# Performance work log

Measured on AMD Instinct MI355X. Metric: run time of the kernel, lower is better.

The kernel has to match this reference:

```python
import jax, jax.numpy as jnp
import numpy as np

N = 4096       # nodes
NFEAT = 256    # feature dim
NCLASS = 16
E = 65536      # edges = N * avg_degree(16)
NLAYER = 4
ALPHA = 0.5    # blancealpha (non-trainable)
LAMBDA_1 = 1.0
LAMBDA_2 = 1.0
EPS = 1e-12    # F.normalize eps


def setup_inputs() -> dict:
    key = jax.random.key(0)
    ks = jax.random.split(key, 9)
    feat = jax.random.normal(ks[0], (N, NFEAT), dtype=jnp.float32)
    z0 = jax.random.uniform(ks[1], (N, NFEAT), dtype=jnp.float32)       # torch.rand init of z
    w1 = jax.random.uniform(ks[2], (N, N), dtype=jnp.float32)           # uniform_(0,1)
    EA = jax.random.uniform(ks[3], (N, N), dtype=jnp.float32)           # uniform_(0,1)
    w2_w = jax.random.normal(ks[4], (2 * NFEAT, NCLASS), dtype=jnp.float32) * 0.05
    w2_b = jnp.zeros((NCLASS,), dtype=jnp.float32)
    edge_i = jax.random.randint(ks[5], (E,), 0, N, dtype=jnp.int32)
    edge_j = jax.random.randint(ks[6], (E,), 0, N, dtype=jnp.int32)
    edge_val = jax.random.uniform(ks[7], (E,), dtype=jnp.float32)
    # dense adjacency from the sparse edge list (coalesce -> duplicate indices sum)
    adj = jnp.zeros((N, N), dtype=jnp.float32).at[edge_i, edge_j].add(edge_val)
    # w22 = ones with zeros at edge positions (as in __init__)
    w22 = jnp.ones((N, N), dtype=jnp.float32).at[edge_i, edge_j].set(0.0)
    return dict(feat=feat, z0=z0, w1=w1, EA=EA, w2_w=w2_w, w2_b=w2_b,
                adj=adj, w22=w22, edge_val=edge_val, edge_i=edge_i, edge_j=edge_j)


def reference(feat, z0, w1, EA, w2_w, w2_b, adj, w22, edge_val, edge_i, edge_j):
    n = feat.shape[0]
    y = feat                      # y starts as feat
    z = z0                        # torch.rand init, passed in for determinism
    EP = jnp.ones((n, n), dtype=feat.dtype)
    masked_EA = ALPHA * EA * w22  # constant across layers
    for _ in range(NLAYER):
        # dropout is identity in eval mode (training=False)
        A = adj * EP + masked_EA            # [n, n]
        yyT = y @ y.T                       # [n, n] (reused; same values as the two torch.mm calls)
        temp = EP.T @ y + A @ y - yyT @ y   # [n, nfeat]
        temp = jax.nn.sigmoid(w1 @ temp)
        y_n = (LAMBDA_2 / 2) * temp + feat
        z_n = z - A @ z                     # (I - A) @ z
        # ans(z, adj): edgewise ||z_i - z_j|| * adj_val scattered to dense
        P = jnp.linalg.norm(z[edge_i] - z[edge_j], axis=1) * edge_val   # [E]
        M = jnp.zeros((n, n), dtype=z.dtype).at[edge_i, edge_j].add(P)
        EP = (LAMBDA_2 * (yyT - masked_EA) - LAMBDA_1 * 0.5 * M) / LAMBDA_2
        y, z = y_n, z_n
    # F.normalize(p=2, dim=1)
    y = y / jnp.maximum(jnp.linalg.norm(y, axis=1, keepdims=True), EPS)
    z = z / jnp.maximum(jnp.linalg.norm(z, axis=1, keepdims=True), EPS)
    p = jnp.concatenate([z, y], axis=1)     # [n, 2*nfeat]
    logits = p @ w2_w + w2_b
    return jax.nn.log_softmax(logits, axis=1)
```

## Files before the change

kernel.cpp:

```cpp
#include <hip/hip_runtime.h>

#define Nn 4096
#define Ff 256
#define NCLS 16
#define Ne 65536
#define TSZ 262144
#define NF (Nn*Ff)
#define NNx (Nn*Nn)
#define KS 8

typedef unsigned short u16;
typedef unsigned int u32;
typedef __attribute__((ext_vector_type(8))) short short8;
typedef __attribute__((ext_vector_type(4))) float float4v;

__device__ __forceinline__ float bfh(u16 u){ return __uint_as_float(((u32)u)<<16); }
__device__ __forceinline__ u16 f2bf(float f){
    u32 u = __float_as_uint(f);
    return (u16)((u + 0x7FFFu + ((u>>16)&1u)) >> 16);
}
__device__ __forceinline__ void gload16(const u16* g, u16* l){
    __builtin_amdgcn_global_load_lds(
        (const __attribute__((address_space(1))) u32*)(const void*)g,
        (__attribute__((address_space(3))) u32*)(void*)l, 16, 0, 0);
}

__device__ float g_yA[NF], g_yB[NF], g_zA[NF], g_zB[NF], g_t1[NF], g_T1[NF];
__device__ float g_G[Ff*Ff], g_col[Ff], g_P[Ne], g_cc[Ne], g_hV[TSZ];
__device__ float g_pb[(size_t)KS*NF];
__device__ u32 g_hK[TSZ], g_slot[Ne];
__device__ int g_cntI[Nn], g_cntJ[Nn], g_rpI[Nn+1], g_rpJ[Nn+1], g_fI[Nn], g_fJ[Nn];
__device__ int g_lI[Ne], g_lJ[Ne];
__device__ __align__(16) u16 g_w1h[NNx], g_w1l[NNx];
__device__ __align__(16) u16 g_meh[NNx], g_mel[NNx];
__device__ __align__(16) u16 g_mth[NNx], g_mtl[NNx];
__device__ __align__(16) u16 g_xAh[NF], g_xAl[NF];
__device__ __align__(16) u16 g_xBh[NF], g_xBl[NF];
__device__ __align__(16) u16 g_x2h[NF], g_x2l[NF];
__device__ __align__(16) u16 g_yhA[NF], g_ylA[NF];
__device__ __align__(16) u16 g_yhB[NF], g_ylB[NF];
__device__ __align__(16) u16 g_gth[Ff*Ff], g_gtl[Ff*Ff];

__global__ __launch_bounds__(256) void k_copy(float* dst, const float* src, int n){
    int i = blockIdx.x*256 + threadIdx.x;
    if (i < n) dst[i] = src[i];
}
__global__ __launch_bounds__(256) void k_zero(float* p, int n){
    int i = blockIdx.x*256 + threadIdx.x;
    if (i < n) p[i] = 0.f;
}
__global__ __launch_bounds__(256) void k_zeroi(int* p, int n){
    int i = blockIdx.x*256 + threadIdx.x;
    if (i < n) p[i] = 0;
}
__global__ __launch_bounds__(256) void k_fillc(float* p, float v, int n){
    int i = blockIdx.x*256 + threadIdx.x;
    if (i < n) p[i] = v;
}
__global__ __launch_bounds__(256) void k_hkeys_clear(u32* K){
    int i = blockIdx.x*256 + threadIdx.x;
    if (i < TSZ) K[i] = 0xFFFFFFFFu;
}
__global__ __launch_bounds__(256) void k_hsetup(u32* K, u32* slot, const int* ei, const int* ej){
    int e = blockIdx.x*256 + threadIdx.x;
    if (e >= Ne) return;
    u32 key = ((u32)ei[e] << 12) | (u32)ej[e];
    u32 h = (key * 2654435761u) & (TSZ-1);
    for (;;){
        u32 old = atomicCAS(&K[h], 0xFFFFFFFFu, key);
        if (old == 0xFFFFFFFFu || old == key){ slot[e] = h; break; }
        h = (h+1) & (TSZ-1);
    }
}
__global__ __launch_bounds__(256) void k_hacc(float* V, const float* P, const u32* slot){
    int e = blockIdx.x*256 + threadIdx.x;
    if (e < Ne) atomicAdd(&V[slot[e]], P[e]);
}

__global__ __launch_bounds__(256) void k_count(int* cntI, int* cntJ, const int* ei, const int* ej){
    int e = blockIdx.x*256 + threadIdx.x;
    if (e < Ne){ atomicAdd(&cntI[ei[e]], 1); atomicAdd(&cntJ[ej[e]], 1); }
}
__global__ __launch_bounds__(1024) void k_scan(const int* cnt, int* rp){
    __shared__ int s[1024];
    int t = threadIdx.x, b = t*4;
    int a0 = cnt[b], a1 = cnt[b+1], a2 = cnt[b+2], a3 = cnt[b+3];
    int sum = a0+a1+a2+a3;
    s[t] = sum; __syncthreads();
    for (int o = 1; o < 1024; o <<= 1){
        int v = (t >= o) ? s[t-o] : 0;
        __syncthreads();
        s[t] += v;
        __syncthreads();
    }
    int excl = s[t] - sum;
    rp[b] = excl; rp[b+1] = excl+a0; rp[b+2] = excl+a0+a1; rp[b+3] = excl+a0+a1+a2;
    if (t == 1023) rp[4096] = s[1023];
}
__global__ __launch_bounds__(256) void k_fillcsr(const int* rpI, const int* rpJ, int* fI, int* fJ,
                                                 int* lI, int* lJ, const int* ei, const int* ej){
    int e = blockIdx.x*256 + threadIdx.x;
    if (e >= Ne) return;
    int i = ei[e], j = ej[e];
    lI[rpI[i] + atomicAdd(&fI[i], 1)] = e;
    lJ[rpJ[j] + atomicAdd(&fJ[j], 1)] = e;
}

__global__ __launch_bounds__(256) void k_split(u16* hi, u16* lo, const float* w){
    int i = blockIdx.x*256 + threadIdx.x;
    float v = w[i];
    u16 h = f2bf(v); hi[i] = h; lo[i] = f2bf(v - bfh(h));
}
__global__ __launch_bounds__(256) void k_splitME2(u16* meh, u16* mel, u16* mth, u16* mtl,
                                                  const float* ea, const float* w22){
    __shared__ float T[64][65];
    int r0 = blockIdx.y*64, c0 = blockIdx.x*64;
    int c = threadIdx.x & 63, rr = threadIdx.x >> 6;
    for (int q = 0; q < 16; ++q){
        int r = q*4 + rr;
        size_t idx = (size_t)(r0+r)*Nn + c0 + c;
        float v = 0.5f*ea[idx]*w22[idx];
        T[r][c] = v;
        u16 h = f2bf(v); meh[idx] = h; mel[idx] = f2bf(v - bfh(h));
    }
    __syncthreads();
    for (int q = 0; q < 16; ++q){
        int r = q*4 + rr;
        float v = T[c][r];
        size_t o = (size_t)(c0+r)*Nn + r0 + c;
        u16 h = f2bf(v); mth[o] = h; mtl[o] = f2bf(v - bfh(h));
    }
}
__global__ __launch_bounds__(256) void k_splitXT(u16* hi, u16* lo, const float* X){
    __shared__ float T[64][65];
    int r0 = blockIdx.y*64, c0 = blockIdx.x*64;
    int c = threadIdx.x & 63, rr = threadIdx.x >> 6;
    for (int q = 0; q < 16; ++q){
        int r = q*4 + rr;
        T[r][c] = X[(size_t)(r0+r)*Ff + c0 + c];
    }
    __syncthreads();
    for (int q = 0; q < 16; ++q){
        int r = q*4 + rr;
        float v = T[c][r];
        size_t o = (size_t)(c0+r)*Nn + r0 + c;
        u16 h = f2bf(v); hi[o] = h; lo[o] = f2bf(v - bfh(h));
    }
}
__global__ __launch_bounds__(256) void k_splitGT(u16* hi, u16* lo, const float* Gm){
    __shared__ float T[64][65];
    int r0 = blockIdx.y*64, c0 = blockIdx.x*64;
    int c = threadIdx.x & 63, rr = threadIdx.x >> 6;
    for (int q = 0; q < 16; ++q){
        int r = q*4 + rr;
        T[r][c] = Gm[(r0+r)*Ff + c0 + c];
    }
    __syncthreads();
    for (int q = 0; q < 16; ++q){
        int r = q*4 + rr;
        float v = T[c][r];
        int o = (c0+r)*Ff + r0 + c;
        u16 h = f2bf(v); hi[o] = h; lo[o] = f2bf(v - bfh(h));
    }
}

__device__ __forceinline__ void mm_tile(
    const u16* __restrict__ Ahp, const u16* __restrict__ Alp,
    const u16* __restrict__ Bhp, const u16* __restrict__ Blp,
    size_t sA, size_t sB, int i0, int j0, int k0,
    u16* LAh, u16* LAl, u16* LBh, u16* LBl,
    float4v* acc, int lane, int w)
{
    const int g1 = w*64 + lane;
    const int g2 = g1 + 256;
    const int r1 = g1>>3, p1 = g1&7, r2 = g2>>3, p2 = g2&7;
    const size_t a1 = (size_t)(i0+r1)*sA + (size_t)(k0 + ((p1 ^ (r1&7))<<3));
    const size_t a2 = (size_t)(i0+r2)*sA + (size_t)(k0 + ((p2 ^ (r2&7))<<3));
    const size_t b1 = (size_t)(j0+r1)*sB + (size_t)(k0 + ((p1 ^ (r1&7))<<3));
// ... 12 lines not shown
    const int aswz = arow & 7;
    #pragma unroll
    for (int kk = 0; kk < 2; ++kk){
        const int ch = kk*4 + (lane>>4);
        short8 ah = *(const short8*)(LAh + arow*64 + ((ch ^ aswz)<<3));
        short8 al = *(const short8*)(LAl + arow*64 + ((ch ^ aswz)<<3));
        #pragma unroll
        for (int c = 0; c < 4; ++c){
            const int brow = c*16 + (lane&15);
            const int bo = brow*64 + ((ch ^ (brow&7))<<3);
            short8 bh = *(const short8*)(LBh + bo);
            short8 bl = *(const short8*)(LBl + bo);
            acc[c] = __builtin_amdgcn_mfma_f32_16x16x32_bf16(ah, bh, acc[c], 0,0,0);
            acc[c] = __builtin_amdgcn_mfma_f32_16x16x32_bf16(ah, bl, acc[c], 0,0,0);
            acc[c] = __builtin_amdgcn_mfma_f32_16x16x32_bf16(al, bh, acc[c], 0,0,0);
        }
    }
}

template<int V>
__global__ __launch_bounds__(256) void k_mm(float* __restrict__ out,
        const u16* __restrict__ Ahp, const u16* __restrict__ Alp,
        const u16* __restrict__ Bhp, const u16* __restrict__ Blp,
        size_t sA, size_t sB, int nkt,
        const float* __restrict__ aux1){
    __shared__ u16 LAh[4096], LAl[4096], LBh[4096], LBl[4096];
    const int tid = threadIdx.x, lane = tid & 63, w = tid >> 6;
    const int j0 = blockIdx.x*64, i0 = blockIdx.y*64;
    float4v acc[4];
    #pragma unroll
    for (int c = 0; c < 4; ++c) acc[c] = (float4v){0.f,0.f,0.f,0.f};
    for (int kt = 0; kt < nkt; ++kt)
        mm_tile(Ahp, Alp, Bhp, Blp, sA, sB, i0, j0, kt*64, LAh, LAl, LBh, LBl, acc, lane, w);
    #pragma unroll
    for (int c = 0; c < 4; ++c)
        #pragma unroll
        for (int r = 0; r < 4; ++r){
            int grow = i0 + w*16 + (lane>>4)*4 + r;
            int gcol = j0 + c*16 + (lane&15);
            size_t idx = (size_t)grow*Ff + gcol;
            float v = acc[c][r];
            if constexpr (V == 3) out[idx] = aux1[idx] - v;
            if constexpr (V == 4) out[idx] = aux1[gcol] - v;
            if constexpr (V == 5) out[idx] = v;
        }
}

__global__ __launch_bounds__(256) void k_gram_mm(float* __restrict__ G,
        const u16* __restrict__ Ahp, const u16* __restrict__ Alp,
        const u16* __restrict__ Bhp, const u16* __restrict__ Blp){
    __shared__ u16 LAh[4096], LAl[4096], LBh[4096], LBl[4096];
    const int tid = threadIdx.x, lane = tid & 63, w = tid >> 6;
    const int j0 = blockIdx.x*64, i0 = blockIdx.y*64, kb = blockIdx.z*256;
    float4v acc[4];
    #pragma unroll
    for (int c = 0; c < 4; ++c) acc[c] = (float4v){0.f,0.f,0.f,0.f};
    for (int kt = 0; kt < 4; ++kt)
        mm_tile(Ahp, Alp, Bhp, Blp, (size_t)Nn, (size_t)Nn, i0, j0, kb + kt*64, LAh, LAl, LBh, LBl, acc, lane, w);
    #pragma unroll
    for (int c = 0; c < 4; ++c)
        #pragma unroll
        for (int r = 0; r < 4; ++r){
            int grow = i0 + w*16 + (lane>>4)*4 + r;
            int gcol = j0 + c*16 + (lane&15);
            atomicAdd(&G[grow*Ff + gcol], acc[c][r]);
        }
}

__global__ __launch_bounds__(512) void k_mmB(float* __restrict__ pb,
        const u16* __restrict__ Ahp, const u16* __restrict__ Alp,
        const u16* __restrict__ Bhp, const u16* __restrict__ Blp){
    __shared__ u16 LAh[4096], LAl[4096], LBh[16384], LBl[16384];
    const int tid = threadIdx.x, lane = tid & 63, w = tid >> 6;
    const int z = blockIdx.x, i0 = blockIdx.y*64;
    const int wr = w >> 2, wc = w & 3;
    float4v acc[2][4];
    #pragma unroll
    for (int m = 0; m < 2; ++m)
        #pragma unroll
        for (int n = 0; n < 4; ++n) acc[m][n] = (float4v){0.f,0.f,0.f,0.f};

    const int ra = tid >> 3, pa = tid & 7;
    const size_t aoff = (size_t)(i0+ra)*Nn + (size_t)((pa ^ (ra&7))<<3);

    for (int kt = 0; kt < 8; ++kt){
        const int k0 = z*512 + kt*64;
        __syncthreads();
        gload16(Ahp + aoff + k0, LAh + tid*8);
        gload16(Alp + aoff + k0, LAl + tid*8);
        #pragma unroll
        for (int it = 0; it < 4; ++it){
            int g = it*512 + tid;
            int r = g >> 3, p = g & 7;
            size_t b = (size_t)r*Nn + (size_t)(k0 + ((p ^ (r&7))<<3));
            gload16(Bhp + b, LBh + g*8);
            gload16(Blp + b, LBl + g*8);
        }
        __syncthreads();
        #pragma unroll
        for (int kk = 0; kk < 2; ++kk){
            const int ch = kk*4 + (lane>>4);
            short8 ah0, ah1, al0, al1;
            {
                const int arow = wr*32 + (lane&15);
                const int ao = arow*64 + ((ch ^ (arow&7))<<3);
                ah0 = *(const short8*)(LAh + ao);
                al0 = *(const short8*)(LAl + ao);
            }
            {
                const int arow = wr*32 + 16 + (lane&15);
                const int ao = arow*64 + ((ch ^ (arow&7))<<3);
                ah1 = *(const short8*)(LAh + ao);
                al1 = *(const short8*)(LAl + ao);
            }
            #pragma unroll
            for (int n = 0; n < 4; ++n){
                const int bcol = wc*64 + n*16 + (lane&15);
                const int bo = bcol*64 + ((ch ^ (bcol&7))<<3);
                short8 bh = *(const short8*)(LBh + bo);
                short8 bl = *(const short8*)(LBl + bo);
                acc[0][n] = __builtin_amdgcn_mfma_f32_16x16x32_bf16(ah0, bh, acc[0][n], 0,0,0);
                acc[0][n] = __builtin_amdgcn_mfma_f32_16x16x32_bf16(ah0, bl, acc[0][n], 0,0,0);
                acc[0][n] = __builtin_amdgcn_mfma_f32_16x16x32_bf16(al0, bh, acc[0][n], 0,0,0);
                acc[1][n] = __builtin_amdgcn_mfma_f32_16x16x32_bf16(ah1, bh, acc[1][n], 0,0,0);
                acc[1][n] = __builtin_amdgcn_mfma_f32_16x16x32_bf16(ah1, bl, acc[1][n], 0,0,0);
                acc[1][n] = __builtin_amdgcn_mfma_f32_16x16x32_bf16(al1, bh, acc[1][n], 0,0,0);
            }
        }
    }
    float* op = pb + (size_t)z*NF;
    #pragma unroll
    for (int m = 0; m < 2; ++m)
        #pragma unroll
        for (int n = 0; n < 4; ++n)
            #pragma unroll
            for (int r = 0; r < 4; ++r){
                int row = i0 + wr*32 + m*16 + (lane>>4)*4 + r;
                int col = wc*64 + n*16 + (lane&15);
                op[(size_t)row*Ff + col] = acc[m][n][r];
            }
}

template<int V>
__global__ __launch_bounds__(256) void k_red(float* __restrict__ out, const float* __restrict__ pb,
                                             const float* __restrict__ aux, u16* __restrict__ oh,
                                             u16* __restrict__ ol){
    size_t i = (size_t)blockIdx.x*256 + threadIdx.x;
    float s = 0.f;
    #pragma unroll
    for (int zz = 0; zz < KS; ++zz) s += pb[(size_t)zz*NF + i];
    if constexpr (V == 0) out[i] += s;
    if constexpr (V == 1) out[i] -= s;
    if constexpr (V == 2){
        float v = aux[i] + 0.5f*(1.f/(1.f+expf(-s)));
        out[i] = v;
        u16 h = f2bf(v); oh[i] = h; ol[i] = f2bf(v - bfh(h));
    }
    if constexpr (V == 3) out[i] = aux[i] - s;
}

__global__ __launch_bounds__(256) void k_csrT(float* __restrict__ t1, const float* __restrict__ y,
        const float* __restrict__ cc, const float* __restrict__ P,
        const int* __restrict__ rpI, const int* __restrict__ lI, const int* __restrict__ ej,
        const int* __restrict__ rpJ, const int* __restrict__ lJ, const int* __restrict__ ei,
        int useM){
    const int r = blockIdx.x, f = threadIdx.x;
    float acc = 0.f;
    const int b0 = rpI[r], b1 = rpI[r+1];
    for (int p = b0; p < b1; ++p){
        int e = lI[p];
        acc += cc[e] * y[(size_t)ej[e]*Ff + f];
    }
    if (useM){
        const int c0 = rpJ[r], c1 = rpJ[r+1];
        for (int p = c0; p < c1; ++p){
            int e = lJ[p];
            acc -= 0.5f * P[e] * y[(size_t)ei[e]*Ff + f];
        }
    }
    t1[(size_t)r*Ff + f] += acc;
}
__global__ __launch_bounds__(256) void k_csrZ(float* __restrict__ zn, const float* __restrict__ z,
        const float* __restrict__ cc,
        const int* __restrict__ rpI, const int* __restrict__ lI, const int* __restrict__ ej){
    const int r = blockIdx.x, f = threadIdx.x;
    float acc = 0.f;
    const int b0 = rpI[r], b1 = rpI[r+1];
    for (int p = b0; p < b1; ++p){
        int e = lI[p];
        acc += cc[e] * z[(size_t)ej[e]*Ff + f];
    }
    zn[(size_t)r*Ff + f] -= acc;
}

__global__ __launch_bounds__(256) void k_colsum(float* col, const float* __restrict__ y){
    int j = threadIdx.x;
    int r0 = blockIdx.x*64;
    float s = 0.f;
    for (int i = 0; i < 64; ++i) s += y[(size_t)(r0+i)*Ff + j];
    atomicAdd(&col[j], s);
}

__global__ __launch_bounds__(256) void k_p(float* __restrict__ P, const float* __restrict__ z,
        const int* __restrict__ ei, const int* __restrict__ ej, const float* __restrict__ ev){
    int e = blockIdx.x*4 + (threadIdx.x >> 6);
    int lane = threadIdx.x & 63;
    int i = ei[e], j = ej[e];
    float s = 0.f;
    #pragma unroll
    for (int q = 0; q < 4; ++q){
        int f = lane + q*64;
        float d = z[(size_t)i*Ff + f] - z[(size_t)j*Ff + f];
        s += d*d;
    }
    #pragma unroll
    for (int o = 32; o; o >>= 1) s += __shfl_xor(s, o);
    if (lane == 0) P[e] = sqrtf(s) * ev[e];
}
__global__ __launch_bounds__(256) void k_ep(float* __restrict__ c, const float* __restrict__ y,
        const int* __restrict__ ei, const int* __restrict__ ej, const float* __restrict__ ev,
        const float* __restrict__ V, const u32* __restrict__ slot){
    int e = blockIdx.x*4 + (threadIdx.x >> 6);
    int lane = threadIdx.x & 63;
    int i = ei[e], j = ej[e];
    float s = 0.f;
    #pragma unroll
    for (int q = 0; q < 4; ++q){
        int f = lane + q*64;
        s += y[(size_t)i*Ff + f] * y[(size_t)j*Ff + f];
    }
    #pragma unroll
    for (int o = 32; o; o >>= 1) s += __shfl_xor(s, o);
    if (lane == 0) c[e] = ev[e] * (s - 0.5f * V[slot[e]]);
}

__global__ __launch_bounds__(256) void k_head(float* __restrict__ out, const float* __restrict__ y,
                                              const float* __restrict__ z, const float* __restrict__ w2w,
                                              const float* __restrict__ w2b){
    const int node = blockIdx.x, t = threadIdx.x;
    float yv = y[(size_t)node*Ff + t], zv = z[(size_t)node*Ff + t];
// ... 46 lines not shown
                              void* d_out, int out_size, void* d_ws, size_t ws_size,
                              hipStream_t stream){
    const float* feat = (const float*)d_in[0];
    const float* z0i  = (const float*)d_in[1];
    const float* w1p  = (const float*)d_in[2];
    const float* EAp  = (const float*)d_in[3];
    const float* w2w  = (const float*)d_in[4];
    const float* w2b  = (const float*)d_in[5];
    const float* w22p = (const float*)d_in[7];
    const float* evp  = (const float*)d_in[8];
    const int* ei   = (const int*)d_in[9];
    const int* ej   = (const int*)d_in[10];
    float* out = (float*)d_out;

    int ok = (n_in == 11) && (out_size == Nn*NCLS)
           && in_sizes[0]==NF && in_sizes[1]==NF && in_sizes[2]==NNx && in_sizes[3]==NNx
           && in_sizes[4]==2*Ff*NCLS && in_sizes[5]==NCLS && in_sizes[6]==NNx && in_sizes[7]==NNx
           && in_sizes[8]==Ne && in_sizes[9]==Ne && in_sizes[10]==Ne;
    if (!ok){
        k_fillc<<<(out_size+255)/256, 256, 0, stream>>>(out, -100.0f, out_size);
        return;
    }

    float *yA,*yB,*zA,*zB,*t1,*T1,*G,*col,*P,*cc,*hV,*pb; u32 *hK,*slot;
    int *cntI,*cntJ,*rpI,*rpJ,*fI,*fJ,*lI,*lJ;
    u16 *w1h,*w1l,*meh,*mel,*mth,*mtl,*xAh,*xAl,*xBh,*xBl,*x2h,*x2l,*yhA,*ylA,*yhB,*ylB,*gth,*gtl;
    hipGetSymbolAddress((void**)&yA,  HIP_SYMBOL(g_yA));
    hipGetSymbolAddress((void**)&yB,  HIP_SYMBOL(g_yB));
    hipGetSymbolAddress((void**)&zA,  HIP_SYMBOL(g_zA));
    hipGetSymbolAddress((void**)&zB,  HIP_SYMBOL(g_zB));
    hipGetSymbolAddress((void**)&t1,  HIP_SYMBOL(g_t1));
    hipGetSymbolAddress((void**)&T1,  HIP_SYMBOL(g_T1));
    hipGetSymbolAddress((void**)&G,   HIP_SYMBOL(g_G));
    hipGetSymbolAddress((void**)&col, HIP_SYMBOL(g_col));
    hipGetSymbolAddress((void**)&P,   HIP_SYMBOL(g_P));
    hipGetSymbolAddress((void**)&cc,  HIP_SYMBOL(g_cc));
    hipGetSymbolAddress((void**)&hV,  HIP_SYMBOL(g_hV));
    hipGetSymbolAddress((void**)&pb,  HIP_SYMBOL(g_pb));
    hipGetSymbolAddress((void**)&hK,  HIP_SYMBOL(g_hK));
    hipGetSymbolAddress((void**)&slot,HIP_SYMBOL(g_slot));
    hipGetSymbolAddress((void**)&cntI,HIP_SYMBOL(g_cntI));
    hipGetSymbolAddress((void**)&cntJ,HIP_SYMBOL(g_cntJ));
    hipGetSymbolAddress((void**)&rpI, HIP_SYMBOL(g_rpI));
    hipGetSymbolAddress((void**)&rpJ, HIP_SYMBOL(g_rpJ));
    hipGetSymbolAddress((void**)&fI,  HIP_SYMBOL(g_fI));
    hipGetSymbolAddress((void**)&fJ,  HIP_SYMBOL(g_fJ));
    hipGetSymbolAddress((void**)&lI,  HIP_SYMBOL(g_lI));
    hipGetSymbolAddress((void**)&lJ,  HIP_SYMBOL(g_lJ));
    hipGetSymbolAddress((void**)&w1h, HIP_SYMBOL(g_w1h));
    hipGetSymbolAddress((void**)&w1l, HIP_SYMBOL(g_w1l));
    hipGetSymbolAddress((void**)&meh, HIP_SYMBOL(g_meh));
    hipGetSymbolAddress((void**)&mel, HIP_SYMBOL(g_mel));
    hipGetSymbolAddress((void**)&mth, HIP_SYMBOL(g_mth));
    hipGetSymbolAddress((void**)&mtl, HIP_SYMBOL(g_mtl));
    hipGetSymbolAddress((void**)&xAh, HIP_SYMBOL(g_xAh));
    hipGetSymbolAddress((void**)&xAl, HIP_SYMBOL(g_xAl));
    hipGetSymbolAddress((void**)&xBh, HIP_SYMBOL(g_xBh));
    hipGetSymbolAddress((void**)&xBl, HIP_SYMBOL(g_xBl));
    hipGetSymbolAddress((void**)&x2h, HIP_SYMBOL(g_x2h));
    hipGetSymbolAddress((void**)&x2l, HIP_SYMBOL(g_x2l));
    hipGetSymbolAddress((void**)&yhA, HIP_SYMBOL(g_yhA));
    hipGetSymbolAddress((void**)&ylA, HIP_SYMBOL(g_ylA));
    hipGetSymbolAddress((void**)&yhB, HIP_SYMBOL(g_yhB));
    hipGetSymbolAddress((void**)&ylB, HIP_SYMBOL(g_ylB));
    hipGetSymbolAddress((void**)&gth, HIP_SYMBOL(g_gth));
    hipGetSymbolAddress((void**)&gtl, HIP_SYMBOL(g_gtl));

    const dim3 gG(Ff/64, Nn/64);
    const dim3 gXT(Ff/64, Nn/64);
    const dim3 gME(Nn/64, Nn/64);
    const dim3 gGT(Ff/64, Ff/64);
    const dim3 gGram(4, 4, 16);
    const dim3 gB(KS, Nn/64);

    k_split  <<<NNx/256, 256, 0, stream>>>(w1h, w1l, w1p);
    k_splitME2<<<gME, 256, 0, stream>>>(meh, mel, mth, mtl, EAp, w22p);
    k_copy<<<NF/256, 256, 0, stream>>>(yA, feat, NF);
    k_copy<<<NF/256, 256, 0, stream>>>(zA, z0i, NF);
    k_copy<<<Ne/256, 256, 0, stream>>>(cc, evp, Ne);
    k_split  <<<NF/256, 256, 0, stream>>>(yhA, ylA, yA);
    k_splitXT<<<gXT, 256, 0, stream>>>(xAh, xAl, yA);
    k_hkeys_clear<<<TSZ/256, 256, 0, stream>>>(hK);
    k_hsetup<<<Ne/256, 256, 0, stream>>>(hK, slot, ei, ej);
    k_zeroi<<<Nn/256, 256, 0, stream>>>(cntI, Nn);
    k_zeroi<<<Nn/256, 256, 0, stream>>>(cntJ, Nn);
    k_count<<<Ne/256, 256, 0, stream>>>(cntI, cntJ, ei, ej);
    k_scan<<<1, 1024, 0, stream>>>(cntI, rpI);
    k_scan<<<1, 1024, 0, stream>>>(cntJ, rpJ);
    k_zeroi<<<Nn/256, 256, 0, stream>>>(fI, Nn);
    k_zeroi<<<Nn/256, 256, 0, stream>>>(fJ, Nn);
    k_fillcsr<<<Ne/256, 256, 0, stream>>>(rpI, rpJ, fI, fJ, lI, lJ, ei, ej);

    float *y = yA, *yn = yB, *z = zA, *zn = zB;
    for (int t = 1; t <= 4; ++t){
        k_zero<<<Ff*Ff/256, 256, 0, stream>>>(G, Ff*Ff);
        k_gram_mm<<<gGram, 256, 0, stream>>>(G, xAh, xAl, xAh, xAl);
        k_splitGT<<<gGT, 256, 0, stream>>>(gth, gtl, G);
        if (t == 1){
            k_zero<<<1, 256, 0, stream>>>(col, Ff);
            k_colsum<<<64, 256, 0, stream>>>(col, y);
            k_mm<4><<<gG, 256, 0, stream>>>(t1, yhA, ylA, gth, gtl, (size_t)Ff, (size_t)Ff, 4, col);
        } else {
            k_mm<3><<<gG, 256, 0, stream>>>(t1, yhA, ylA, gth, gtl, (size_t)Ff, (size_t)Ff, 4, T1);
        }
        k_csrT<<<Nn, 256, 0, stream>>>(t1, y, cc, P, rpI, lI, ej, rpJ, lJ, ei, (t >= 2) ? 1 : 0);
        k_mmB<<<gB, 512, 0, stream>>>(pb, meh, mel, xAh, xAl);
        k_red<0><<<NF/256, 256, 0, stream>>>(t1, pb, nullptr, nullptr, nullptr);
        if (t >= 2){
            k_mmB<<<gB, 512, 0, stream>>>(pb, mth, mtl, xAh, xAl);
            k_red<1><<<NF/256, 256, 0, stream>>>(t1, pb, nullptr, nullptr, nullptr);
        }
        k_splitXT<<<gXT, 256, 0, stream>>>(x2h, x2l, t1);
        k_mmB<<<gB, 512, 0, stream>>>(pb, w1h, w1l, x2h, x2l);
        k_red<2><<<NF/256, 256, 0, stream>>>(yn, pb, feat, yhB, ylB);
        k_splitXT<<<gXT, 256, 0, stream>>>(x2h, x2l, z);
        k_mmB<<<gB, 512, 0, stream>>>(pb, meh, mel, x2h, x2l);
        k_red<3><<<NF/256, 256, 0, stream>>>(zn, pb, z, nullptr, nullptr);
        k_csrZ<<<Nn, 256, 0, stream>>>(zn, z, cc, rpI, lI, ej);
        if (t < 4){
            k_p<<<Ne/4, 256, 0, stream>>>(P, z, ei, ej, evp);
            k_zero<<<TSZ/256, 256, 0, stream>>>(hV, TSZ);
            k_hacc<<<Ne/256, 256, 0, stream>>>(hV, P, slot);
            k_ep<<<Ne/4, 256, 0, stream>>>(cc, y, ei, ej, evp, hV, slot);
            k_splitXT<<<gXT, 256, 0, stream>>>(xBh, xBl, yn);
            k_zero<<<Ff*Ff/256, 256, 0, stream>>>(G, Ff*Ff);
            k_gram_mm<<<gGram, 256, 0, stream>>>(G, xAh, xAl, xBh, xBl);
            k_splitGT<<<gGT, 256, 0, stream>>>(gth, gtl, G);
            k_mm<5><<<gG, 256, 0, stream>>>(T1, yhA, ylA, gth, gtl, (size_t)Ff, (size_t)Ff, 4, nullptr);
        }
        float* tmp;
        tmp = y; y = yn; yn = tmp;
        tmp = z; z = zn; zn = tmp;
        u16* tu;
        tu = xAh; xAh = xBh; xBh = tu;
        tu = xAl; xAl = xBl; xBl = tu;
        tu = yhA; yhA = yhB; yhB = tu;
        tu = ylA; ylA = ylB; ylB = tu;
    }
    k_head<<<Nn, 256, 0, stream>>>(out, y, z, w2w, w2b);
}
```

Baseline: 1.368 ms.

## Retile big GEMM with double-buffered 128x128 tiles and fuse reductions with splits

Rewrites the large N×N-by-N×F GEMM kernel to use 128x128 output tiles with double-buffered LDS staging and a split-K of 4 instead of 8. This cuts LDS reloads of the N×N operand and the partial-buffer traffic. Several other changes come with it. The reduction kernels now also do the transposed bf16 hi/lo split, and the z and y CSR passes are fused into one kernel. The Gram matrix is written as per-slice partials summed during the split, removing atomics and zeroing. Copies are dropped, and the init splits are vectorized with float4. Larger tiles mean fewer blocks and more LDS per block, so occupancy may drop.

```diff
diff --git a/kernel.cpp b/kernel.cpp
--- a/kernel.cpp
+++ b/kernel.cpp
@@ -7,7 +7,7 @@
 #define TSZ 262144
 #define NF (Nn*Ff)
 #define NNx (Nn*Nn)
-#define KS 8
+#define KS 4
 
 typedef unsigned short u16;
 typedef unsigned int u32;
@@ -26,7 +26,7 @@
 }
 
 __device__ float g_yA[NF], g_yB[NF], g_zA[NF], g_zB[NF], g_t1[NF], g_T1[NF];
-__device__ float g_G[Ff*Ff], g_col[Ff], g_P[Ne], g_cc[Ne], g_hV[TSZ];
+__device__ float g_Gp[16*Ff*Ff], g_col[Ff], g_P[Ne], g_cc[Ne], g_hV[TSZ];
 __device__ float g_pb[(size_t)KS*NF];
 __device__ u32 g_hK[TSZ], g_slot[Ne];
 __device__ int g_cntI[Nn], g_cntJ[Nn], g_rpI[Nn+1], g_rpJ[Nn+1], g_fI[Nn], g_fJ[Nn];
@@ -34,17 +34,12 @@
 __device__ __align__(16) u16 g_w1h[NNx], g_w1l[NNx];
 __device__ __align__(16) u16 g_meh[NNx], g_mel[NNx];
 __device__ __align__(16) u16 g_mth[NNx], g_mtl[NNx];
-__device__ __align__(16) u16 g_xAh[NF], g_xAl[NF];
-__device__ __align__(16) u16 g_xBh[NF], g_xBl[NF];
-__device__ __align__(16) u16 g_x2h[NF], g_x2l[NF];
-__device__ __align__(16) u16 g_yhA[NF], g_ylA[NF];
-__device__ __align__(16) u16 g_yhB[NF], g_ylB[NF];
+__device__ __align__(16) u16 g_x0h[NF], g_x0l[NF], g_x1h[NF], g_x1l[NF];
+__device__ __align__(16) u16 g_zt0h[NF], g_zt0l[NF], g_zt1h[NF], g_zt1l[NF];
+__device__ __align__(16) u16 g_yr0h[NF], g_yr0l[NF], g_yr1h[NF], g_yr1l[NF];
+__device__ __align__(16) u16 g_tth[NF], g_ttl[NF];
 __device__ __align__(16) u16 g_gth[Ff*Ff], g_gtl[Ff*Ff];
 
-__global__ __launch_bounds__(256) void k_copy(float* dst, const float* src, int n){
-    int i = blockIdx.x*256 + threadIdx.x;
-    if (i < n) dst[i] = src[i];
-}
 __global__ __launch_bounds__(256) void k_zero(float* p, int n){
     int i = blockIdx.x*256 + threadIdx.x;
     if (i < n) p[i] = 0.f;
@@ -71,10 +66,6 @@
         if (old == 0xFFFFFFFFu || old == key){ slot[e] = h; break; }
         h = (h+1) & (TSZ-1);
     }
-}
-__global__ __launch_bounds__(256) void k_hacc(float* V, const float* P, const u32* slot){
-    int e = blockIdx.x*256 + threadIdx.x;
-    if (e < Ne) atomicAdd(&V[slot[e]], P[e]);
 }
 
 __global__ __launch_bounds__(256) void k_count(int* cntI, int* cntJ, const int* ei, const int* ej){
@@ -106,29 +97,47 @@
     lJ[rpJ[j] + atomicAdd(&fJ[j], 1)] = e;
 }
 
-__global__ __launch_bounds__(256) void k_split(u16* hi, u16* lo, const float* w){
+__global__ __launch_bounds__(256) void k_split4(ushort4* hi, ushort4* lo, const float4* w, int n4){
     int i = blockIdx.x*256 + threadIdx.x;
-    float v = w[i];
-    u16 h = f2bf(v); hi[i] = h; lo[i] = f2bf(v - bfh(h));
+    if (i >= n4) return;
+    float4 v = w[i];
+    ushort4 h, l;
+    h.x = f2bf(v.x); l.x = f2bf(v.x - bfh(h.x));
+    h.y = f2bf(v.y); l.y = f2bf(v.y - bfh(h.y));
+    h.z = f2bf(v.z); l.z = f2bf(v.z - bfh(h.z));
+    h.w = f2bf(v.w); l.w = f2bf(v.w - bfh(h.w));
+    hi[i] = h; lo[i] = l;
 }
 __global__ __launch_bounds__(256) void k_splitME2(u16* meh, u16* mel, u16* mth, u16* mtl,
                                                   const float* ea, const float* w22){
     __shared__ float T[64][65];
     int r0 = blockIdx.y*64, c0 = blockIdx.x*64;
-    int c = threadIdx.x & 63, rr = threadIdx.x >> 6;
-    for (int q = 0; q < 16; ++q){
-        int r = q*4 + rr;
-        size_t idx = (size_t)(r0+r)*Nn + c0 + c;
-        float v = 0.5f*ea[idx]*w22[idx];
-        T[r][c] = v;
-        u16 h = f2bf(v); meh[idx] = h; mel[idx] = f2bf(v - bfh(h));
-    }
-    __syncthreads();
-    for (int q = 0; q < 16; ++q){
-        int r = q*4 + rr;
-        float v = T[c][r];
-        size_t o = (size_t)(c0+r)*Nn + r0 + c;
-        u16 h = f2bf(v); mth[o] = h; mtl[o] = f2bf(v - bfh(h));
+    int c4 = threadIdx.x & 15, rr = threadIdx.x >> 4;
+    for (int q = 0; q < 4; ++q){
+        int r = q*16 + rr;
+        size_t idx = (size_t)(r0+r)*Nn + c0 + c4*4;
+        float4 e4 = *(const float4*)(ea + idx);
+        float4 w4 = *(const float4*)(w22 + idx);
+        float v0 = 0.5f*e4.x*w4.x, v1 = 0.5f*e4.y*w4.y, v2 = 0.5f*e4.z*w4.z, v3 = 0.5f*e4.w*w4.w;
+        ushort4 h, l;
+        h.x = f2bf(v0); l.x = f2bf(v0 - bfh(h.x));
+        h.y = f2bf(v1); l.y = f2bf(v1 - bfh(h.y));
+        h.z = f2bf(v2); l.z = f2bf(v2 - bfh(h.z));
+        h.w = f2bf(v3); l.w = f2bf(v3 - bfh(h.w));
+        *(ushort4*)(meh + idx) = h; *(ushort4*)(mel + idx) = l;
+        T[r][c4*4+0] = v0; T[r][c4*4+1] = v1; T[r][c4*4+2] = v2; T[r][c4*4+3] = v3;
+    }
+    __syncthreads();
+    for (int q = 0; q < 4; ++q){
+        int oc = q*16 + rr;
+        float v0 = T[c4*4+0][oc], v1 = T[c4*4+1][oc], v2 = T[c4*4+2][oc], v3 = T[c4*4+3][oc];
+        ushort4 h, l;
+        h.x = f2bf(v0); l.x = f2bf(v0 - bfh(h.x));
+        h.y = f2bf(v1); l.y = f2bf(v1 - bfh(h.y));
+        h.z = f2bf(v2); l.z = f2bf(v2 - bfh(h.z));
+        h.w = f2bf(v3); l.w = f2bf(v3 - bfh(h.w));
+        size_t o = (size_t)(c0+oc)*Nn + r0 + c4*4;
+        *(ushort4*)(mth + o) = h; *(ushort4*)(mtl + o) = l;
     }
 }
 __global__ __launch_bounds__(256) void k_splitXT(u16* hi, u16* lo, const float* X){
@@ -147,13 +156,16 @@
         u16 h = f2bf(v); hi[o] = h; lo[o] = f2bf(v - bfh(h));
     }
 }
-__global__ __launch_bounds__(256) void k_splitGT(u16* hi, u16* lo, const float* Gm){
+__global__ __launch_bounds__(256) void k_splitGT(u16* hi, u16* lo, const float* Gp){
     __shared__ float T[64][65];
     int r0 = blockIdx.y*64, c0 = blockIdx.x*64;
     int c = threadIdx.x & 63, rr = threadIdx.x >> 6;
     for (int q = 0; q < 16; ++q){
         int r = q*4 + rr;
-        T[r][c] = Gm[(r0+r)*Ff + c0 + c];
+        float v = 0.f;
+        #pragma unroll
+        for (int z = 0; z < 16; ++z) v += Gp[z*(Ff*Ff) + (r0+r)*Ff + c0 + c];
+        T[r][c] = v;
     }
     __syncthreads();
     for (int q = 0; q < 16; ++q){
@@ -212,7 +224,6 @@
 __global__ __launch_bounds__(256) void k_mm(float* __restrict__ out,
         const u16* __restrict__ Ahp, const u16* __restrict__ Alp,
         const u16* __restrict__ Bhp, const u16* __restrict__ Blp,
-        size_t sA, size_t sB, int nkt,
         const float* __restrict__ aux1){
     __shared__ u16 LAh[4096], LAl[4096], LBh[4096], LBl[4096];
     const int tid = threadIdx.x, lane = tid & 63, w = tid >> 6;
@@ -220,8 +231,8 @@
     float4v acc[4];
     #pragma unroll
     for (int c = 0; c < 4; ++c) acc[c] = (float4v){0.f,0.f,0.f,0.f};
-    for (int kt = 0; kt < nkt; ++kt)
-        mm_tile(Ahp, Alp, Bhp, Blp, sA, sB, i0, j0, kt*64, LAh, LAl, LBh, LBl, acc, lane, w);
+    for (int kt = 0; kt < 4; ++kt)
+        mm_tile(Ahp, Alp, Bhp, Blp, (size_t)Ff, (size_t)Ff, i0, j0, kt*64, LAh, LAl, LBh, LBl, acc, lane, w);
     #pragma unroll
     for (int c = 0; c < 4; ++c)
         #pragma unroll
@@ -236,7 +247,7 @@
         }
 }
 
-__global__ __launch_bounds__(256) void k_gram_mm(float* __restrict__ G,
+__global__ __launch_bounds__(256) void k_gram_mm(float* __restrict__ Gp,
         const u16* __restrict__ Ahp, const u16* __restrict__ Alp,
         const u16* __restrict__ Bhp, const u16* __restrict__ Blp){
     __shared__ u16 LAh[4096], LAl[4096], LBh[4096], LBl[4096];
@@ -247,78 +258,83 @@
     for (int c = 0; c < 4; ++c) acc[c] = (float4v){0.f,0.f,0.f,0.f};
     for (int kt = 0; kt < 4; ++kt)
         mm_tile(Ahp, Alp, Bhp, Blp, (size_t)Nn, (size_t)Nn, i0, j0, kb + kt*64, LAh, LAl, LBh, LBl, acc, lane, w);
+    float* op = Gp + (size_t)blockIdx.z*(Ff*Ff);
     #pragma unroll
     for (int c = 0; c < 4; ++c)
         #pragma unroll
         for (int r = 0; r < 4; ++r){
             int grow = i0 + w*16 + (lane>>4)*4 + r;
             int gcol = j0 + c*16 + (lane&15);
-            atomicAdd(&G[grow*Ff + gcol], acc[c][r]);
+            op[grow*Ff + gcol] = acc[c][r];
         }
 }
 
 __global__ __launch_bounds__(512) void k_mmB(float* __restrict__ pb,
-        const u16* __restrict__ Ahp, const u16* __restrict__ Alp,
-        const u16* __restrict__ Bhp, const u16* __restrict__ Blp){
-    __shared__ u16 LAh[4096], LAl[4096], LBh[16384], LBl[16384];
+        const u16* __restrict__ Ah, const u16* __restrict__ Al,
+        const u16* __restrict__ Bh, const u16* __restrict__ Bl){
+    __shared__ u16 LA[2][2][8192];
+    __shared__ u16 LB[2][2][8192];
     const int tid = threadIdx.x, lane = tid & 63, w = tid >> 6;
-    const int z = blockIdx.x, i0 = blockIdx.y*64;
-    const int wr = w >> 2, wc = w & 3;
+    const int j0 = blockIdx.x*128, i0 = blockIdx.y*128;
+    const int kbase = blockIdx.z*1024;
+    const int wr = w >> 1, wc = w & 1;
     float4v acc[2][4];
     #pragma unroll
     for (int m = 0; m < 2; ++m)
         #pragma unroll
         for (int n = 0; n < 4; ++n) acc[m][n] = (float4v){0.f,0.f,0.f,0.f};
 
-    const int ra = tid >> 3, pa = tid & 7;
-    const size_t aoff = (size_t)(i0+ra)*Nn + (size_t)((pa ^ (ra&7))<<3);
-
-    for (int kt = 0; kt < 8; ++kt){
-        const int k0 = z*512 + kt*64;
+    const int srow = tid >> 3, sp = tid & 7;
+    const size_t aoff0 = (size_t)(i0 + srow)*Nn + (size_t)((sp ^ (srow&7))<<3);
+    const size_t aoff1 = aoff0 + (size_t)64*Nn;
+    const size_t boff0 = (size_t)(j0 + srow)*Nn + (size_t)((sp ^ (srow&7))<<3);
+    const size_t boff1 = boff0 + (size_t)64*Nn;
+    const int d0 = tid*8, d1 = tid*8 + 4096;
+
+#define STAGE(B, K0) { \
+    gload16(Ah + aoff0 + (K0), &LA[B][0][d0]); \
+    gload16(Ah + aoff1 + (K0), &LA[B][0][d1]); \
+    gload16(Al + aoff0 + (K0), &LA[B][1][d0]); \
+    gload16(Al + aoff1 + (K0), &LA[B][1][d1]); \
+    gload16(Bh + boff0 + (K0), &LB[B][0][d0]); \
+    gload16(Bh + boff1 + (K0), &LB[B][0][d1]); \
+    gload16(Bl + boff0 + (K0), &LB[B][1][d0]); \
+    gload16(Bl + boff1 + (K0), &LB[B][1][d1]); }
+
+#define COMPUTE(B) { \
+    _Pragma("unroll") \
+    for (int kk = 0; kk < 2; ++kk){ \
+        const int ch = kk*4 + (lane>>4); \
+        short8 ah0, al0, ah1, al1; \
+        { int ar = wr*32 + (lane&15); int ao = ar*64 + ((ch ^ (ar&7))<<3); \
+          ah0 = *(const short8*)&LA[B][0][ao]; al0 = *(const short8*)&LA[B][1][ao]; } \
+        { int ar = wr*32 + 16 + (lane&15); int ao = ar*64 + ((ch ^ (ar&7))<<3); \
+          ah1 = *(const short8*)&LA[B][0][ao]; al1 = *(const short8*)&LA[B][1][ao]; } \
+        _Pragma("unroll") \
+        for (int n = 0; n < 4; ++n){ \
+            int bc = wc*64 + n*16 + (lane&15); int bo = bc*64 + ((ch ^ (bc&7))<<3); \
+            short8 bh = *(const short8*)&LB[B][0][bo]; \
+            short8 bl = *(const short8*)&LB[B][1][bo]; \
+            acc[0][n] = __builtin_amdgcn_mfma_f32_16x16x32_bf16(ah0, bh, acc[0][n], 0,0,0); \
+            acc[0][n] = __builtin_amdgcn_mfma_f32_16x16x32_bf16(ah0, bl, acc[0][n], 0,0,0); \
+            acc[0][n] = __builtin_amdgcn_mfma_f32_16x16x32_bf16(al0, bh, acc[0][n], 0,0,0); \
+            acc[1][n] = __builtin_amdgcn_mfma_f32_16x16x32_bf16(ah1, bh, acc[1][n], 0,0,0); \
+            acc[1][n] = __builtin_amdgcn_mfma_f32_16x16x32_bf16(ah1, bl, acc[1][n], 0,0,0); \
+            acc[1][n] = __builtin_amdgcn_mfma_f32_16x16x32_bf16(al1, bh, acc[1][n], 0,0,0); \
+        } \
+    } }
+
+    STAGE(0, kbase)
+    __syncthreads();
+    for (int kt = 0; kt < 16; ++kt){
+        if (kt < 15) STAGE((kt+1)&1, kbase + (kt+1)*64)
+        COMPUTE(kt&1)
         __syncthreads();
-        gload16(Ahp + aoff + k0, LAh + tid*8);
-        gload16(Alp + aoff + k0, LAl + tid*8);
-        #pragma unroll
-        for (int it = 0; it < 4; ++it){
-            int g = it*512 + tid;
-            int r = g >> 3, p = g & 7;
-            size_t b = (size_t)r*Nn + (size_t)(k0 + ((p ^ (r&7))<<3));
-            gload16(Bhp + b, LBh + g*8);
-            gload16(Blp + b, LBl + g*8);
-        }
-        __syncthreads();
-        #pragma unroll
-        for (int kk = 0; kk < 2; ++kk){
-            const int ch = kk*4 + (lane>>4);
-            short8 ah0, ah1, al0, al1;
-            {
-                const int arow = wr*32 + (lane&15);
-                const int ao = arow*64 + ((ch ^ (arow&7))<<3);
-                ah0 = *(const short8*)(LAh + ao);
-                al0 = *(const short8*)(LAl + ao);
-            }
-            {
-                const int arow = wr*32 + 16 + (lane&15);
-                const int ao = arow*64 + ((ch ^ (arow&7))<<3);
-                ah1 = *(const short8*)(LAh + ao);
-                al1 = *(const short8*)(LAl + ao);
-            }
-            #pragma unroll
-            for (int n = 0; n < 4; ++n){
-                const int bcol = wc*64 + n*16 + (lane&15);
-                const int bo = bcol*64 + ((ch ^ (bcol&7))<<3);
-                short8 bh = *(const short8*)(LBh + bo);
-                short8 bl = *(const short8*)(LBl + bo);
-                acc[0][n] = __builtin_amdgcn_mfma_f32_16x16x32_bf16(ah0, bh, acc[0][n], 0,0,0);
-                acc[0][n] = __builtin_amdgcn_mfma_f32_16x16x32_bf16(ah0, bl, acc[0][n], 0,0,0);
-                acc[0][n] = __builtin_amdgcn_mfma_f32_16x16x32_bf16(al0, bh, acc[0][n], 0,0,0);
-                acc[1][n] = __builtin_amdgcn_mfma_f32_16x16x32_bf16(ah1, bh, acc[1][n], 0,0,0);
-                acc[1][n] = __builtin_amdgcn_mfma_f32_16x16x32_bf16(ah1, bl, acc[1][n], 0,0,0);
-                acc[1][n] = __builtin_amdgcn_mfma_f32_16x16x32_bf16(al1, bh, acc[1][n], 0,0,0);
-            }
-        }
-    }
-    float* op = pb + (size_t)z*NF;
+    }
+#undef STAGE
+#undef COMPUTE
+
+    float* op = pb + (size_t)blockIdx.z*NF;
     #pragma unroll
     for (int m = 0; m < 2; ++m)
         #pragma unroll
@@ -326,61 +342,69 @@
             #pragma unroll
             for (int r = 0; r < 4; ++r){
                 int row = i0 + wr*32 + m*16 + (lane>>4)*4 + r;
-                int col = wc*64 + n*16 + (lane&15);
+                int col = j0 + wc*64 + n*16 + (lane&15);
                 op[(size_t)row*Ff + col] = acc[m][n][r];
             }
 }
 
-template<int V>
-__global__ __launch_bounds__(256) void k_red(float* __restrict__ out, const float* __restrict__ pb,
-                                             const float* __restrict__ aux, u16* __restrict__ oh,
-                                             u16* __restrict__ ol){
-    size_t i = (size_t)blockIdx.x*256 + threadIdx.x;
-    float s = 0.f;
-    #pragma unroll
-    for (int zz = 0; zz < KS; ++zz) s += pb[(size_t)zz*NF + i];
-    if constexpr (V == 0) out[i] += s;
-    if constexpr (V == 1) out[i] -= s;
-    if constexpr (V == 2){
-        float v = aux[i] + 0.5f*(1.f/(1.f+expf(-s)));
-        out[i] = v;
-        u16 h = f2bf(v); oh[i] = h; ol[i] = f2bf(v - bfh(h));
-    }
-    if constexpr (V == 3) out[i] = aux[i] - s;
-}
-
-__global__ __launch_bounds__(256) void k_csrT(float* __restrict__ t1, const float* __restrict__ y,
+template<int V, int DOSPLIT>
+__global__ __launch_bounds__(256) void k_redT(float* __restrict__ out, const float* __restrict__ pb,
+        const float* __restrict__ aux, u16* __restrict__ rh, u16* __restrict__ rl,
+        u16* __restrict__ th, u16* __restrict__ tl){
+    __shared__ float T[64][65];
+    const int c0 = blockIdx.x*64, r0 = blockIdx.y*64;
+    const int c = threadIdx.x & 63, rr = threadIdx.x >> 6;
+    for (int q = 0; q < 16; ++q){
+        int row = q*4 + rr;
+        size_t idx = (size_t)(r0+row)*Ff + c0 + c;
+        float s = pb[idx] + pb[NF+idx] + pb[2*(size_t)NF+idx] + pb[3*(size_t)NF+idx];
+        float val;
+        if constexpr (V == 0) val = out[idx] + s;
+        if constexpr (V == 1) val = out[idx] - s;
+        if constexpr (V == 2) val = aux[idx] + 0.5f*(1.f/(1.f+expf(-s)));
+        if constexpr (V == 3) val = aux[idx] - s;
+        out[idx] = val;
+        if constexpr (V == 2){
+            u16 h = f2bf(val); rh[idx] = h; rl[idx] = f2bf(val - bfh(h));
+        }
+        if constexpr (DOSPLIT) T[row][c] = val;
+    }
+    if constexpr (DOSPLIT){
+        __syncthreads();
+        for (int q = 0; q < 16; ++q){
+            int r = q*4 + rr;
+            float v = T[c][r];
+            size_t o = (size_t)(c0+r)*Nn + r0 + c;
+            u16 h = f2bf(v); th[o] = h; tl[o] = f2bf(v - bfh(h));
+        }
+    }
+}
+
+__global__ __launch_bounds__(256) void k_csrTZ(float* __restrict__ t1, float* __restrict__ zn,
+        const float* __restrict__ y, const float* __restrict__ z,
         const float* __restrict__ cc, const float* __restrict__ P,
         const int* __restrict__ rpI, const int* __restrict__ lI, const int* __restrict__ ej,
         const int* __restrict__ rpJ, const int* __restrict__ lJ, const int* __restrict__ ei,
         int useM){
     const int r = blockIdx.x, f = threadIdx.x;
-    float acc = 0.f;
+    float at = 0.f, az = 0.f;
     const int b0 = rpI[r], b1 = rpI[r+1];
     for (int p = b0; p < b1; ++p){
         int e = lI[p];
-        acc += cc[e] * y[(size_t)ej[e]*Ff + f];
+        float ce = cc[e];
+        int j = ej[e];
+        at += ce * y[(size_t)j*Ff + f];
+        az += ce * z[(size_t)j*Ff + f];
     }
     if (useM){
         const int c0 = rpJ[r], c1 = rpJ[r+1];
         for (int p = c0; p < c1; ++p){
             int e = lJ[p];
-            acc -= 0.5f * P[e] * y[(size_t)ei[e]*Ff + f];
-        }
-    }
-    t1[(size_t)r*Ff + f] += acc;
-}
-__global__ __launch_bounds__(256) void k_csrZ(float* __restrict__ zn, const float* __restrict__ z,
-        const float* __restrict__ cc,
-        const int* __restrict__ rpI, const int* __restrict__ lI, const int* __restrict__ ej){
-    const int r = blockIdx.x, f = threadIdx.x;
-    float acc = 0.f;
-    const int b0 = rpI[r], b1 = rpI[r+1];
-    for (int p = b0; p < b1; ++p){
-        int e = lI[p];
-        acc += cc[e] * z[(size_t)ej[e]*Ff + f];
-    }
-    zn[(size_t)r*Ff + f] -= acc;
+            at -= 0.5f * P[e] * y[(size_t)ei[e]*Ff + f];
+        }
+    }
+    t1[(size_t)r*Ff + f] += at;
+    zn[(size_t)r*Ff + f] -= az;
 }
 
 __global__ __launch_bounds__(256) void k_colsum(float* col, const float* __restrict__ y){
@@ -391,8 +415,9 @@
     atomicAdd(&col[j], s);
 }
 
-__global__ __launch_bounds__(256) void k_p(float* __restrict__ P, const float* __restrict__ z,
-        const int* __restrict__ ei, const int* __restrict__ ej, const float* __restrict__ ev){
+__global__ __launch_bounds__(256) void k_pacc(float* __restrict__ P, float* __restrict__ hV,
+        const float* __restrict__ z, const int* __restrict__ ei, const int* __restrict__ ej,
+        const float* __restrict__ ev, const u32* __restrict__ slot){
     int e = blockIdx.x*4 + (threadIdx.x >> 6);
     int lane = threadIdx.x & 63;
     int i = ei[e], j = ej[e];
@@ -405,7 +430,11 @@
     }
     #pragma unroll
     for (int o = 32; o; o >>= 1) s += __shfl_xor(s, o);
-    if (lane == 0) P[e] = sqrtf(s) * ev[e];
+    if (lane == 0){
+        float v = sqrtf(s) * ev[e];
+        P[e] = v;
+        atomicAdd(&hV[slot[e]], v);
+    }
 }
 __global__ __launch_bounds__(256) void k_ep(float* __restrict__ c, const float* __restrict__ y,
         const int* __restrict__ ei, const int* __restrict__ ej, const float* __restrict__ ev,
@@ -498,16 +527,17 @@
         return;
     }
 
-    float *yA,*yB,*zA,*zB,*t1,*T1,*G,*col,*P,*cc,*hV,*pb; u32 *hK,*slot;
+    float *yA,*yB,*zA,*zB,*t1,*T1,*Gp,*col,*P,*cc,*hV,*pb; u32 *hK,*slot;
     int *cntI,*cntJ,*rpI,*rpJ,*fI,*fJ,*lI,*lJ;
-    u16 *w1h,*w1l,*meh,*mel,*mth,*mtl,*xAh,*xAl,*xBh,*xBl,*x2h,*x2l,*yhA,*ylA,*yhB,*ylB,*gth,*gtl;
+    u16 *w1h,*w1l,*meh,*mel,*mth,*mtl,*gth,*gtl,*tth,*ttl;
+    u16 *xh[2],*xl[2],*zth[2],*ztl[2],*yrh[2],*yrl[2];
     hipGetSymbolAddress((void**)&yA,  HIP_SYMBOL(g_yA));
     hipGetSymbolAddress((void**)&yB,  HIP_SYMBOL(g_yB));
     hipGetSymbolAddress((void**)&zA,  HIP_SYMBOL(g_zA));
     hipGetSymbolAddress((void**)&zB,  HIP_SYMBOL(g_zB));
     hipGetSymbolAddress((void**)&t1,  HIP_SYMBOL(g_t1));
     hipGetSymbolAddress((void**)&T1,  HIP_SYMBOL(g_T1));
-    hipGetSymbolAddress((void**)&G,   HIP_SYMBOL(g_G));
+    hipGetSymbolAddress((void**)&Gp,  HIP_SYMBOL(g_Gp));
     hipGetSymbolAddress((void**)&col, HIP_SYMBOL(g_col));
     hipGetSymbolAddress((void**)&P,   HIP_SYMBOL(g_P));
     hipGetSymbolAddress((void**)&cc,  HIP_SYMBOL(g_cc));
@@ -529,33 +559,36 @@
     hipGetSymbolAddress((void**)&mel, HIP_SYMBOL(g_mel));
     hipGetSymbolAddress((void**)&mth, HIP_SYMBOL(g_mth));
     hipGetSymbolAddress((void**)&mtl, HIP_SYMBOL(g_mtl));
-    hipGetSymbolAddress((void**)&xAh, HIP_SYMBOL(g_xAh));
-    hipGetSymbolAddress((void**)&xAl, HIP_SYMBOL(g_xAl));
-    hipGetSymbolAddress((void**)&xBh, HIP_SYMBOL(g_xBh));
-    hipGetSymbolAddress((void**)&xBl, HIP_SYMBOL(g_xBl));
-    hipGetSymbolAddress((void**)&x2h, HIP_SYMBOL(g_x2h));
-    hipGetSymbolAddress((void**)&x2l, HIP_SYMBOL(g_x2l));
-    hipGetSymbolAddress((void**)&yhA, HIP_SYMBOL(g_yhA));
-    hipGetSymbolAddress((void**)&ylA, HIP_SYMBOL(g_ylA));
-    hipGetSymbolAddress((void**)&yhB, HIP_SYMBOL(g_yhB));
-    hipGetSymbolAddress((void**)&ylB, HIP_SYMBOL(g_ylB));
     hipGetSymbolAddress((void**)&gth, HIP_SYMBOL(g_gth));
     hipGetSymbolAddress((void**)&gtl, HIP_SYMBOL(g_gtl));
-
-    const dim3 gG(Ff/64, Nn/64);
+    hipGetSymbolAddress((void**)&tth, HIP_SYMBOL(g_tth));
+    hipGetSymbolAddress((void**)&ttl, HIP_SYMBOL(g_ttl));
+    hipGetSymbolAddress((void**)&xh[0], HIP_SYMBOL(g_x0h));
+    hipGetSymbolAddress((void**)&xl[0], HIP_SYMBOL(g_x0l));
+    hipGetSymbolAddress((void**)&xh[1], HIP_SYMBOL(g_x1h));
+    hipGetSymbolAddress((void**)&xl[1], HIP_SYMBOL(g_x1l));
+    hipGetSymbolAddress((void**)&zth[0], HIP_SYMBOL(g_zt0h));
+    hipGetSymbolAddress((void**)&ztl[0], HIP_SYMBOL(g_zt0l));
+    hipGetSymbolAddress((void**)&zth[1], HIP_SYMBOL(g_zt1h));
+    hipGetSymbolAddress((void**)&ztl[1], HIP_SYMBOL(g_zt1l));
+    hipGetSymbolAddress((void**)&yrh[0], HIP_SYMBOL(g_yr0h));
+    hipGetSymbolAddress((void**)&yrl[0], HIP_SYMBOL(g_yr0l));
+    hipGetSymbolAddress((void**)&yrh[1], HIP_SYMBOL(g_yr1h));
+    hipGetSymbolAddress((void**)&yrl[1], HIP_SYMBOL(g_yr1l));
+
+    const dim3 gSmall(Ff/64, Nn/64);
     const dim3 gXT(Ff/64, Nn/64);
     const dim3 gME(Nn/64, Nn/64);
     const dim3 gGT(Ff/64, Ff/64);
     const dim3 gGram(4, 4, 16);
-    const dim3 gB(KS, Nn/64);
-
-    k_split  <<<NNx/256, 256, 0, stream>>>(w1h, w1l, w1p);
+    const dim3 gB(2, Nn/128, KS);
+    const dim3 gRed(Ff/64, Nn/64);
+
+    k_split4<<<NNx/4/256, 256, 0, stream>>>((ushort4*)w1h, (ushort4*)w1l, (const float4*)w1p, NNx/4);
     k_splitME2<<<gME, 256, 0, stream>>>(meh, mel, mth, mtl, EAp, w22p);
-    k_copy<<<NF/256, 256, 0, stream>>>(yA, feat, NF);
-    k_copy<<<NF/256, 256, 0, stream>>>(zA, z0i, NF);
-    k_copy<<<Ne/256, 256, 0, stream>>>(cc, evp, Ne);
-    k_split  <<<NF/256, 256, 0, stream>>>(yhA, ylA, yA);
-    k_splitXT<<<gXT, 256, 0, stream>>>(xAh, xAl, yA);
+    k_split4<<<NF/4/256, 256, 0, stream>>>((ushort4*)yrh[0], (ushort4*)yrl[0], (const float4*)feat, NF/4);
+    k_splitXT<<<gXT, 256, 0, stream>>>(xh[0], xl[0], feat);
+    k_splitXT<<<gXT, 256, 0, stream>>>(zth[0], ztl[0], z0i);
     k_hkeys_clear<<<TSZ/256, 256, 0, stream>>>(hK);
     k_hsetup<<<Ne/256, 256, 0, stream>>>(hK, slot, ei, ej);
     k_zeroi<<<Nn/256, 256, 0, stream>>>(cntI, Nn);
@@ -567,51 +600,49 @@
     k_zeroi<<<Nn/256, 256, 0, stream>>>(fJ, Nn);
     k_fillcsr<<<Ne/256, 256, 0, stream>>>(rpI, rpJ, fI, fJ, lI, lJ, ei, ej);
 
-    float *y = yA, *yn = yB, *z = zA, *zn = zB;
+    const float* yv = feat;  const float* zv = z0i;
     for (int t = 1; t <= 4; ++t){
-        k_zero<<<Ff*Ff/256, 256, 0, stream>>>(G, Ff*Ff);
-        k_gram_mm<<<gGram, 256, 0, stream>>>(G, xAh, xAl, xAh, xAl);
-        k_splitGT<<<gGT, 256, 0, stream>>>(gth, gtl, G);
+        int ri = (t-1) & 1, wi = t & 1;
+        u16 *xhc = xh[ri], *xlc = xl[ri], *xhn = xh[wi], *xln = xl[wi];
+        u16 *zthc = zth[ri], *ztlc = ztl[ri], *zthn = zth[wi], *ztln = ztl[wi];
+        u16 *yrhc = yrh[ri], *yrlc = yrl[ri], *yrhn = yrh[wi], *yrln = yrl[wi];
+        float* yn = (t & 1) ? yA : yB;
+        float* zn = (t & 1) ? zA : zB;
+        const float* ccv = (t == 1) ? evp : cc;
+
+        k_gram_mm<<<gGram, 256, 0, stream>>>(Gp, xhc, xlc, xhc, xlc);
+        k_splitGT<<<gGT, 256, 0, stream>>>(gth, gtl, Gp);
         if (t == 1){
             k_zero<<<1, 256, 0, stream>>>(col, Ff);
-            k_colsum<<<64, 256, 0, stream>>>(col, y);
-            k_mm<4><<<gG, 256, 0, stream>>>(t1, yhA, ylA, gth, gtl, (size_t)Ff, (size_t)Ff, 4, col);
+            k_colsum<<<64, 256, 0, stream>>>(col, yv);
+            k_mm<4><<<gSmall, 256, 0, stream>>>(t1, yrhc, yrlc, gth, gtl, col);
         } else {
-            k_mm<3><<<gG, 256, 0, stream>>>(t1, yhA, ylA, gth, gtl, (size_t)Ff, (size_t)Ff, 4, T1);
-        }
-        k_csrT<<<Nn, 256, 0, stream>>>(t1, y, cc, P, rpI, lI, ej, rpJ, lJ, ei, (t >= 2) ? 1 : 0);
-        k_mmB<<<gB, 512, 0, stream>>>(pb, meh, mel, xAh, xAl);
-        k_red<0><<<NF/256, 256, 0, stream>>>(t1, pb, nullptr, nullptr, nullptr);
-        if (t >= 2){
-            k_mmB<<<gB, 512, 0, stream>>>(pb, mth, mtl, xAh, xAl);
-            k_red<1><<<NF/256, 256, 0, stream>>>(t1, pb, nullptr, nullptr, nullptr);
-        }
-        k_splitXT<<<gXT, 256, 0, stream>>>(x2h, x2l, t1);
-        k_mmB<<<gB, 512, 0, stream>>>(pb, w1h, w1l, x2h, x2l);
-        k_red<2><<<NF/256, 256, 0, stream>>>(yn, pb, feat, yhB, ylB);
-        k_splitXT<<<gXT, 256, 0, stream>>>(x2h, x2l, z);
-        k_mmB<<<gB, 512, 0, stream>>>(pb, meh, mel, x2h, x2l);
-        k_red<3><<<NF/256, 256, 0, stream>>>(zn, pb, z, nullptr, nullptr);
-        k_csrZ<<<Nn, 256, 0, stream>>>(zn, z, cc, rpI, lI, ej);
+            k_mm<3><<<gSmall, 256, 0, stream>>>(t1, yrhc, yrlc, gth, gtl, T1);
+        }
+        k_mmB<<<gB, 512, 0, stream>>>(pb, meh, mel, zthc, ztlc);
+        k_redT<3,0><<<gRed, 256, 0, stream>>>(zn, pb, zv, nullptr, nullptr, nullptr, nullptr);
+        k_csrTZ<<<Nn, 256, 0, stream>>>(t1, zn, yv, zv, ccv, P, rpI, lI, ej, rpJ, lJ, ei, (t >= 2) ? 1 : 0);
+        if (t < 4)
+            k_splitXT<<<gXT, 256, 0, stream>>>(zthn, ztln, zn);
+        k_mmB<<<gB, 512, 0, stream>>>(pb, meh, mel, xhc, xlc);
+        if (t == 1){
+            k_redT<0,1><<<gRed, 256, 0, stream>>>(t1, pb, nullptr, nullptr, nullptr, tth, ttl);
+        } else {
+            k_redT<0,0><<<gRed, 256, 0, stream>>>(t1, pb, nullptr, nullptr, nullptr, nullptr, nullptr);
+            k_mmB<<<gB, 512, 0, stream>>>(pb, mth, mtl, xhc, xlc);
+            k_redT<1,1><<<gRed, 256, 0, stream>>>(t1, pb, nullptr, nullptr, nullptr, tth, ttl);
+        }
+        k_mmB<<<gB, 512, 0, stream>>>(pb, w1h, w1l, tth, ttl);
+        k_redT<2,1><<<gRed, 256, 0, stream>>>(yn, pb, feat, yrhn, yrln, xhn, xln);
         if (t < 4){
-            k_p<<<Ne/4, 256, 0, stream>>>(P, z, ei, ej, evp);
             k_zero<<<TSZ/256, 256, 0, stream>>>(hV, TSZ);
-            k_hacc<<<Ne/256, 256, 0, stream>>>(hV, P, slot);
-            k_ep<<<Ne/4, 256, 0, stream>>>(cc, y, ei, ej, evp, hV, slot);
-            k_splitXT<<<gXT, 256, 0, stream>>>(xBh, xBl, yn);
-            k_zero<<<Ff*Ff/256, 256, 0, stream>>>(G, Ff*Ff);
-            k_gram_mm<<<gGram, 256, 0, stream>>>(G, xAh, xAl, xBh, xBl);
-            k_splitGT<<<gGT, 256, 0, stream>>>(gth, gtl, G);
-            k_mm<5><<<gG, 256, 0, stream>>>(T1, yhA, ylA, gth, gtl, (size_t)Ff, (size_t)Ff, 4, nullptr);
-        }
-        float* tmp;
-        tmp = y; y = yn; yn = tmp;
-        tmp = z; z = zn; zn = tmp;
-        u16* tu;
-        tu = xAh; xAh = xBh; xBh = tu;
-        tu = xAl; xAl = xBl; xBl = tu;
-        tu = yhA; yhA = yhB; yhB = tu;
-        tu = ylA; ylA = ylB; ylB = tu;
-    }
-    k_head<<<Nn, 256, 0, stream>>>(out, y, z, w2w, w2b);
-}
+            k_pacc<<<Ne/4, 256, 0, stream>>>(P, hV, zv, ei, ej, evp, slot);
+            k_ep<<<Ne/4, 256, 0, stream>>>(cc, yv, ei, ej, evp, hV, slot);
+            k_gram_mm<<<gGram, 256, 0, stream>>>(Gp, xhc, xlc, xhn, xln);
+            k_splitGT<<<gGT, 256, 0, stream>>>(gth, gtl, Gp);
+            k_mm<5><<<gSmall, 256, 0, stream>>>(T1, yrhc, yrlc, gth, gtl, nullptr);
+        }
+        yv = yn; zv = zn;
+    }
+    k_head<<<Nn, 256, 0, stream>>>(out, yv, zv, w2w, w2b);
+}
```

Measured after the change: 1.568 ms. +14.6%, slower.
